# Kernel optimization log

Hardware: AMD Instinct MI355X
Metric: run time of the kernel (lower is better)

Reference implementation:

```python
import jax, jax.numpy as jnp
import numpy as np

NHID = 512
PROJ = 64          # fixed 64-dim projection from the source code
N_NODES = 16384
N_CLAIM = 4096
N_EVID = 8192
N_GRAPHS = 64


def setup_inputs() -> dict:
    key = jax.random.key(0)
    ks = jax.random.split(key, 10)
    x = jax.random.normal(ks[0], (N_NODES, NHID), dtype=jnp.float32)
    batch = jnp.sort(jax.random.randint(ks[1], (N_NODES,), 0, N_GRAPHS, dtype=jnp.int64))
    claim_index = jax.random.randint(ks[2], (N_CLAIM,), 0, N_NODES, dtype=jnp.int64)
    evidence_index = jax.random.randint(ks[3], (N_EVID,), 0, N_NODES, dtype=jnp.int64)
    # Linear params (PyTorch Linear: y = x @ W.T + b; store as [in, out] here)
    s_c = 1.0 / np.sqrt(NHID)
    Wc = jax.random.uniform(ks[4], (NHID, PROJ), jnp.float32, -s_c, s_c)
    bc = jax.random.uniform(ks[5], (PROJ,), jnp.float32, -s_c, s_c)
    We = jax.random.uniform(ks[6], (NHID, PROJ), jnp.float32, -s_c, s_c)
    be = jax.random.uniform(ks[7], (PROJ,), jnp.float32, -s_c, s_c)
    s_a = 1.0 / np.sqrt(4 * NHID)
    Wa = jax.random.uniform(ks[8], (4 * NHID, NHID), jnp.float32, -s_a, s_a)
    ba = jax.random.uniform(ks[9], (NHID,), jnp.float32, -s_a, s_a)
    return {"x": x, "batch": batch, "claim_index": claim_index,
            "evidence_index": evidence_index,
            "Wc": Wc, "bc": bc, "We": We, "be": be, "Wa": Wa, "ba": ba}


def reference(x, batch, claim_index, evidence_index, Wc, bc, We, be, Wa, ba):
    claim_batch = batch[claim_index]          # [Nc]
    evidence_batch = batch[evidence_index]    # [Ne]
    # block-diagonal mask: 0 where same graph, -inf otherwise
    same = claim_batch[:, None] == evidence_batch[None, :]
    mask = jnp.where(same, 0.0, -jnp.inf).astype(jnp.float32)  # [Nc, Ne]

    claim = x[claim_index]       # [Nc, nhid]
    evidence = x[evidence_index]  # [Ne, nhid]

    weight_c = claim @ Wc + bc    # [Nc, 64]
    weight_e = evidence @ We + be  # [Ne, 64]
    scores = weight_c @ weight_e.T + mask          # [Nc, Ne]
    attn = jax.nn.softmax(scores, axis=-1)
    claim_new = attn @ evidence                    # [Nc, nhid]

    a = jnp.concatenate([claim, claim_new, claim - claim_new, claim * claim_new], axis=-1)
    a = a @ Wa + ba               # [Nc, nhid]

    # global_mean_pool over claim_batch
    seg_sum = jax.ops.segment_sum(a, claim_batch, num_segments=N_GRAPHS)
    counts = jax.ops.segment_sum(jnp.ones((a.shape[0],), a.dtype), claim_batch,
                                 num_segments=N_GRAPHS)
    res = seg_sum / jnp.maximum(counts, 1.0)[:, None]  # [B, nhid]
    return res
```

## Files before the change

kernel.cpp:

```cpp
#include <hip/hip_runtime.h>
#include <hip/hip_bf16.h>

#define NHID 512
#define PROJ 64
#define NC 4096
#define NEV 8192
#define NG 64
#define NCMAX 128
#define NE_CAP 256
#define DSLICES 4
#define DW 128

typedef __attribute__((ext_vector_type(8))) short s16x8;
typedef __attribute__((ext_vector_type(8))) unsigned short u16x8;
typedef __attribute__((ext_vector_type(4))) float f32x4;

#define P_S_STRIDE 264
#define P_S_BYTES  (NCMAX * P_S_STRIDE * 2)
#define REGB_OFF   P_S_BYTES
#define WE_S_STRIDE 72
#define WC_S_OFF   (REGB_OFF + NE_CAP * WE_S_STRIDE * 2)
#define CN_S_STRIDE 132
#define MISC_OFF   (REGB_OFF + P_S_BYTES)
#define SMEM_BYTES (MISC_OFF + 1536)

static __device__ __forceinline__ unsigned short f2b(float f) {
  union { __hip_bfloat16 h; unsigned short u; } v;
  v.h = __float2bfloat16(f);
  return v.u;
}

template <int NPT>
__device__ __forceinline__ void compact_pairs(
    const int* __restrict__ batch, const int* __restrict__ idx, int g,
    int* __restrict__ off_out, int* __restrict__ cnt_out, int2* __restrict__ pairs) {
  __shared__ int wtot[4], wless[4];
  int t = threadIdx.x, lane = t & 63, w = t >> 6;
  int vals[NPT], nid[NPT];
  int base_i = t * NPT;
  int eq = 0, less = 0;
#pragma unroll
  for (int j = 0; j < NPT; j++) {
    int node = idx[base_i + j];
    int v = batch[node];
    vals[j] = v;
    nid[j] = node;
    eq += (v == g) ? 1 : 0;
    less += (v < g) ? 1 : 0;
  }
  int s = eq;
#pragma unroll
  for (int off = 1; off < 64; off <<= 1) {
    int o = __shfl_up(s, off);
    if (lane >= off) s += o;
  }
  int ls = less;
#pragma unroll
  for (int off = 32; off; off >>= 1) ls += __shfl_xor(ls, off);
  if (lane == 63) wtot[w] = s;
  if (lane == 0) wless[w] = ls;
  __syncthreads();
  int wbase = 0;
#pragma unroll
  for (int k = 0; k < 4; k++)
    if (k < w) wbase += wtot[k];
  int base = wless[0] + wless[1] + wless[2] + wless[3];
  int pos = base + wbase + (s - eq);
#pragma unroll
  for (int j = 0; j < NPT; j++) {
    if (vals[j] == g) pairs[pos++] = make_int2(base_i + j, nid[j]);
  }
  if (t == 255) {
    cnt_out[g] = wbase + s;
    off_out[g] = base;
  }
}

__global__ __launch_bounds__(256) void k_front(
    const float* __restrict__ Wc, const float* __restrict__ We,
    unsigned short* __restrict__ WcT, unsigned short* __restrict__ WeT,
    const int* __restrict__ batch, const int* __restrict__ cidx,
    const int* __restrict__ eidx, int* __restrict__ c_off, int* __restrict__ c_cnt,
    int2* __restrict__ c_pair, int* __restrict__ e_off, int* __restrict__ e_cnt,
    int2* __restrict__ e_pair) {
  int b = blockIdx.x;
  if (b < 16) {
    __shared__ float ts[64][65];
    const float* src = (b < 8) ? Wc : We;
    unsigned short* dst = (b < 8) ? WcT : WeT;
    int k0 = (b & 7) * 64;
    int t = threadIdx.x;
    int c = t & 63, r0 = t >> 6;
#pragma unroll
    for (int p = 0; p < 16; p++) {
      int r = r0 * 16 + p;
      ts[r][c] = src[(size_t)(k0 + r) * 64 + c];
    }
    __syncthreads();
    int n = t >> 2, q = t & 3;
    unsigned short tmp[16];
#pragma unroll
    for (int j = 0; j < 16; j++) tmp[j] = f2b(ts[q * 16 + j][n]);
    u16x8* dp = (u16x8*)(dst + (size_t)n * NHID + k0 + q * 16);
    dp[0] = *(u16x8*)tmp;
    dp[1] = *(u16x8*)(tmp + 8);
  } else if (b < 80) {
    compact_pairs<NC / 256>(batch, cidx, b - 16, c_off, c_cnt, c_pair);
  } else {
    compact_pairs<NEV / 256>(batch, eidx, b - 80, e_off, e_cnt, e_pair);
  }
}

__global__ __launch_bounds__(256) void k_proj(
    const float* __restrict__ x, const int* __restrict__ cidx,
    const int* __restrict__ eidx, const unsigned short* __restrict__ WcT,
    const unsigned short* __restrict__ WeT, const float* __restrict__ bc,
    const float* __restrict__ be, const float* __restrict__ Wa,
    unsigned short* __restrict__ WaT, unsigned short* __restrict__ wcp,
    unsigned short* __restrict__ wep) {
  __shared__ __align__(16) char sm[64 * 65 * 4];
  int b = blockIdx.x;
  int t = threadIdx.x;
  if (b >= 768) {
    int tb = b - 768;
    float(*ts)[65] = (float(*)[65])sm;
    int k0 = (tb >> 3) * 64, n0 = (tb & 7) * 64;
    int c = t & 63, r0 = t >> 6;
#pragma unroll
    for (int p = 0; p < 16; p++) {
      int r = r0 * 16 + p;
      ts[r][c] = Wa[(size_t)(k0 + r) * NHID + n0 + c];
    }
    __syncthreads();
    int n = t >> 2, q = t & 3;
    unsigned short tmp[16];
#pragma unroll
    for (int j = 0; j < 16; j++) tmp[j] = f2b(ts[q * 16 + j][n]);
    u16x8* dp = (u16x8*)(WaT + (size_t)(n0 + n) * (4 * NHID) + k0 + q * 16);
    dp[0] = *(u16x8*)tmp;
    dp[1] = *(u16x8*)(tmp + 8);
    return;
  }
  float(*red)[16][64] = (float(*)[16][64])sm;
  const int* idx; const unsigned short* WT; const float* bias;
  unsigned short* out; int base;
  if (b < NC / 16) { idx = cidx; WT = WcT; bias = bc; out = wcp; base = b * 16; }
  else             { idx = eidx; WT = WeT; bias = be; out = wep; base = (b - NC / 16) * 16; }
  int lane = t & 63, kh = t >> 6;
  int ln = lane & 15, kb = lane >> 4;
  const float* xr = x + (size_t)idx[base + ln] * NHID + kh * 128;
  const unsigned short* wb = WT + kh * 128;
  f32x4 acc[4];
#pragma unroll
  for (int nt = 0; nt < 4; nt++) acc[nt] = (f32x4){0.f, 0.f, 0.f, 0.f};
#pragma unroll
  for (int kt = 0; kt < 4; kt++) {
    int k0 = kt * 32 + kb * 8;
    float4 p0 = *(const float4*)(xr + k0);
    float4 p1 = *(const float4*)(xr + k0 + 4);
    s16x8 a;
    a[0] = (short)f2b(p0.x); a[1] = (short)f2b(p0.y);
    a[2] = (short)f2b(p0.z); a[3] = (short)f2b(p0.w);
    a[4] = (short)f2b(p1.x); a[5] = (short)f2b(p1.y);
    a[6] = (short)f2b(p1.z); a[7] = (short)f2b(p1.w);
#pragma unroll
    for (int nt = 0; nt < 4; nt++) {
      s16x8 bf = *(const s16x8*)(wb + (size_t)(nt * 16 + ln) * NHID + k0);
      acc[nt] = __builtin_amdgcn_mfma_f32_16x16x32_bf16(a, bf, acc[nt], 0, 0, 0);
    }
  }
#pragma unroll
  for (int nt = 0; nt < 4; nt++)
#pragma unroll
    for (int r = 0; r < 4; r++)
      red[kh][kb * 4 + r][nt * 16 + ln] = acc[nt][r];
  __syncthreads();
  for (int i = t; i < 512; i += 256) {
    int row = i >> 5, cp = i & 31;
    int c0 = cp * 2;
    float v0 = red[0][row][c0] + red[1][row][c0] + red[2][row][c0] + red[3][row][c0] + bias[c0];
    float v1 = red[0][row][c0 + 1] + red[1][row][c0 + 1] + red[2][row][c0 + 1] + red[3][row][c0 + 1] + bias[c0 + 1];
    unsigned int pk = (unsigned)f2b(v0) | ((unsigned)f2b(v1) << 16);
    *(unsigned int*)(out + (size_t)(base + row) * PROJ + c0) = pk;
  }
}

__global__ __launch_bounds__(512, 2) void k_attn(
    const float* __restrict__ x, const unsigned short* __restrict__ wcp,
    const unsigned short* __restrict__ wep, const int* __restrict__ c_off,
    const int* __restrict__ c_cnt, const int2* __restrict__ c_pair,
    const int* __restrict__ e_off, const int* __restrict__ e_cnt,
    const int2* __restrict__ e_pair, unsigned short* __restrict__ mcb) {
  __shared__ __align__(16) char smem[SMEM_BYTES];
  unsigned short* P_s  = (unsigned short*)(smem);
  unsigned short* we_s = (unsigned short*)(smem + REGB_OFF);
  unsigned short* wc_s = (unsigned short*)(smem + WC_S_OFF);
  unsigned short* evT  = (unsigned short*)(smem + REGB_OFF);
  unsigned int*   evT32 = (unsigned int*)(smem + REGB_OFF);
  float*          cn_s = (float*)(smem + REGB_OFF);
  float*          pp   = (float*)(smem);
  int* ev_id = (int*)(smem + MISC_OFF);
  int* cl_id = (int*)(smem + MISC_OFF + 1024);

  int g = blockIdx.x >> 2;
  int ds = blockIdx.x & 3;
  int dsbase = ds * DW;
  int t = threadIdx.x, lane = t & 63, w = t >> 6;
  int ln = lane & 15, kb = lane >> 4;

  int ne = min(e_cnt[g], NE_CAP);
  int eoff = e_off[g];
  int ccnt_full = c_cnt[g];
  int nloc = min(ccnt_full, NCMAX);
  int coff = c_off[g];
  if (nloc <= 0) {
    int q = t >> 7, d = t & 127;
    mcb[(size_t)g * 4 * NHID + q * NHID + dsbase + d] = 0;
    return;
  }
  int KT = (ne + 31) >> 5;
  int NT = KT * 2;

  for (int e = t; e < NE_CAP; e += 512)
    ev_id[e] = (e < ne) ? e_pair[eoff + e].y : 0;
  if (t < NCMAX) cl_id[t] = (t < nloc) ? c_pair[coff + t].y : 0;
  {
    int q = t & 7, er = t >> 3;
    for (int base_ = 0; base_ < NE_CAP; base_ += 64) {
      int e = base_ + er;
      u16x8 v = (u16x8){0, 0, 0, 0, 0, 0, 0, 0};
      if (e < ne) v = *(const u16x8*)(wep + (size_t)e_pair[eoff + e].x * PROJ + q * 8);
      *(u16x8*)(we_s + e * WE_S_STRIDE + q * 8) = v;
    }
    for (int base_ = 0; base_ < NCMAX; base_ += 64) {
      int c = base_ + er;
      u16x8 v = (u16x8){0, 0, 0, 0, 0, 0, 0, 0};
      if (c < nloc) v = *(const u16x8*)(wcp + (size_t)c_pair[coff + c].x * PROJ + q * 8);
      *(u16x8*)(wc_s + c * WE_S_STRIDE + q * 8) = v;
    }
  }
  __syncthreads();

  {
    f32x4 sa[16];
#pragma unroll
    for (int i = 0; i < 16; i++) sa[i] = (f32x4){0.f, 0.f, 0.f, 0.f};
    const unsigned short* arow = wc_s + ((w << 4) + ln) * WE_S_STRIDE;
#pragma unroll
    for (int ks = 0; ks < 2; ks++) {
      s16x8 af = *(const s16x8*)(arow + ks * 32 + kb * 8);
#pragma unroll
      for (int nt = 0; nt < 16; nt++) {
        if (nt < NT) {
          s16x8 bf = *(const s16x8*)(we_s + (nt * 16 + ln) * WE_S_STRIDE + ks * 32 + kb * 8);
          sa[nt] = __builtin_amdgcn_mfma_f32_16x16x32_bf16(af, bf, sa[nt], 0, 0, 0);
        }
      }
    }
#pragma unroll
    for (int r = 0; r < 4; r++) {
      int claim = (w << 4) + (kb << 2) + r;
      float mx = -1e30f;
#pragma unroll
      for (int nt = 0; nt < 16; nt++) {
        if (nt < NT) {
          float v = sa[nt][r];
          v = (nt * 16 + ln < ne) ? v : -1e30f;
          sa[nt][r] = v;
          mx = fmaxf(mx, v);
        }
      }
      mx = fmaxf(mx, __shfl_xor(mx, 1));
      mx = fmaxf(mx, __shfl_xor(mx, 2));
      mx = fmaxf(mx, __shfl_xor(mx, 4));
      mx = fmaxf(mx, __shfl_xor(mx, 8));
      float sum = 0.f;
#pragma unroll
      for (int nt = 0; nt < 16; nt++) {
        if (nt < NT) {
          float p = __expf(sa[nt][r] - mx);
          sa[nt][r] = p;
          sum += p;
        }
      }
      sum += __shfl_xor(sum, 1);
      sum += __shfl_xor(sum, 2);
      sum += __shfl_xor(sum, 4);
      sum += __shfl_xor(sum, 8);
      float inv = 1.f / sum;
#pragma unroll
      for (int nt = 0; nt < 16; nt++) {
        if (nt < NT)
          P_s[claim * P_S_STRIDE + nt * 16 + ln] = f2b(sa[nt][r] * inv);
      }
    }
  }
  __syncthreads();

#pragma unroll 4
  for (int pi = w; pi < NE_CAP / 2; pi += 8) {
    int e0 = pi * 2;
    float2 va = make_float2(0.f, 0.f);
    float2 vb = make_float2(0.f, 0.f);
    if (e0 < ne)     va = *(const float2*)(x + (size_t)ev_id[e0] * NHID + dsbase + 2 * lane);
    if (e0 + 1 < ne) vb = *(const float2*)(x + (size_t)ev_id[e0 + 1] * NHID + dsbase + 2 * lane);
    evT32[(2 * lane)     * (P_S_STRIDE / 2) + pi] = (unsigned)f2b(va.x) | ((unsigned)f2b(vb.x) << 16);
    evT32[(2 * lane + 1) * (P_S_STRIDE / 2) + pi] = (unsigned)f2b(va.y) | ((unsigned)f2b(vb.y) << 16);
  }
  __syncthreads();

  int dq4 = (t & 31) * 4;
  int mg = t >> 5;
  float4 cl_r[8];
#pragma unroll
  for (int mi = 0; mi < 8; mi++) {
    int m = mg + mi * 16;
    cl_r[mi] = make_float4(0.f, 0.f, 0.f, 0.f);
    if (m < nloc)
      cl_r[mi] = *(const float4*)(x + (size_t)cl_id[m] * NHID + dsbase + dq4);
  }

  int mw = w >> 1, nw = w & 1;
  int m0 = mw * 32, n0 = nw * 64;
  f32x4 pc[8];
#pragma unroll
  for (int i = 0; i < 8; i++) pc[i] = (f32x4){0.f, 0.f, 0.f, 0.f};
  {
    const unsigned short* prow0 = P_s + (m0 + ln) * P_S_STRIDE + kb * 8;
    const unsigned short* prow1 = prow0 + 16 * P_S_STRIDE;
#pragma unroll
    for (int kt = 0; kt < 8; kt++) {
      if (kt < KT) {
        int k0 = kt * 32;
        s16x8 a0 = *(const s16x8*)(prow0 + k0);
        s16x8 a1 = *(const s16x8*)(prow1 + k0);
#pragma unroll
        for (int nt = 0; nt < 4; nt++) {
          s16x8 bf = *(const s16x8*)(evT + (n0 + nt * 16 + ln) * P_S_STRIDE + k0 + kb * 8);
          pc[nt]     = __builtin_amdgcn_mfma_f32_16x16x32_bf16(a0, bf, pc[nt], 0, 0, 0);
          pc[4 + nt] = __builtin_amdgcn_mfma_f32_16x16x32_bf16(a1, bf, pc[4 + nt], 0, 0, 0);
        }
      }
    }
  }
  __syncthreads();

#pragma unroll
  for (int mi = 0; mi < 2; mi++) {
#pragma unroll
    for (int nt = 0; nt < 4; nt++) {
      f32x4 v = pc[mi * 4 + nt];
#pragma unroll
      for (int r = 0; r < 4; r++)
        cn_s[(m0 + mi * 16 + (kb << 2) + r) * CN_S_STRIDE + n0 + nt * 16 + ln] = v[r];
    }
  }
  __syncthreads();

  {
    float4 scl = make_float4(0.f, 0.f, 0.f, 0.f);
    float4 scn = make_float4(0.f, 0.f, 0.f, 0.f);
    float4 spr = make_float4(0.f, 0.f, 0.f, 0.f);
#pragma unroll
    for (int mi = 0; mi < 8; mi++) {
      int m = mg + mi * 16;
      if (m < nloc) {
        float4 cl = cl_r[mi];
        float4 cn = *(const float4*)(cn_s + m * CN_S_STRIDE + dq4);
        scl.x += cl.x; scl.y += cl.y; scl.z += cl.z; scl.w += cl.w;
        scn.x += cn.x; scn.y += cn.y; scn.z += cn.z; scn.w += cn.w;
        spr.x += cl.x * cn.x; spr.y += cl.y * cn.y;
        spr.z += cl.z * cn.z; spr.w += cl.w * cn.w;
      }
    }
    *(float4*)(pp + mg * 128 + dq4) = scl;
    *(float4*)(pp + 2048 + mg * 128 + dq4) = scn;
    *(float4*)(pp + 4096 + mg * 128 + dq4) = spr;
  }
  __syncthreads();

  {
    int q = t >> 7, d = t & 127;
    float inv = 1.f / (float)max(ccnt_full, 1);
    float v = 0.f;
    if (q == 0) {
#pragma unroll
      for (int mg2 = 0; mg2 < 16; mg2++) v += pp[mg2 * 128 + d];
    } else if (q == 1) {
#pragma unroll
      for (int mg2 = 0; mg2 < 16; mg2++) v += pp[2048 + mg2 * 128 + d];
    } else if (q == 2) {
#pragma unroll
      for (int mg2 = 0; mg2 < 16; mg2++) v += pp[mg2 * 128 + d] - pp[2048 + mg2 * 128 + d];
    } else {
#pragma unroll
      for (int mg2 = 0; mg2 < 16; mg2++) v += pp[4096 + mg2 * 128 + d];
    }
    mcb[(size_t)g * 4 * NHID + q * NHID + dsbase + d] = f2b(v * inv);
  }
}

__global__ __launch_bounds__(512) void k_out(
    const unsigned short* __restrict__ mc, const unsigned short* __restrict__ WaT,
    const float* __restrict__ ba, float* __restrict__ out) {
  __shared__ float red[2][64][16];
  int n0 = blockIdx.x * 16;
  int t = threadIdx.x, lane = t & 63, wv = t >> 6;
  int mh = wv & 3, kh = wv >> 2;
  int ln = lane & 15, kb = lane >> 4;
  f32x4 acc = (f32x4){0.f, 0.f, 0.f, 0.f};
  const unsigned short* arow = mc + (size_t)(mh * 16 + ln) * (4 * NHID) + kh * 1024;
  const unsigned short* wcol = WaT + (size_t)(n0 + ln) * (4 * NHID) + kh * 1024;
#pragma unroll 4
  for (int kt = 0; kt < 32; kt++) {
    int k0 = kt * 32 + kb * 8;
    s16x8 af = *(const s16x8*)(arow + k0);
    s16x8 bf = *(const s16x8*)(wcol + k0);
    acc = __builtin_amdgcn_mfma_f32_16x16x32_bf16(af, bf, acc, 0, 0, 0);
  }
#pragma unroll
  for (int r = 0; r < 4; r++)
    red[kh][mh * 16 + kb * 4 + r][ln] = acc[r];
  __syncthreads();
  for (int i = t; i < 1024; i += 512) {
    int row = i >> 4, col = i & 15;
    out[(size_t)row * NHID + n0 + col] = red[0][row][col] + red[1][row][col] + ba[n0 + col];
  }
}

extern "C" void kernel_launch(void* const* d_in, const int* in_sizes, int n_in,
                              void* d_out, int out_size, void* d_ws, size_t ws_size,
                              hipStream_t stream) {
  const float* x = (const float*)d_in[0];
  const int* batch = (const int*)d_in[1];
  const int* cidx = (const int*)d_in[2];
  const int* eidx = (const int*)d_in[3];
  const float* Wc = (const float*)d_in[4];
  const float* bc = (const float*)d_in[5];
  const float* We = (const float*)d_in[6];
  const float* be = (const float*)d_in[7];
  const float* Wa = (const float*)d_in[8];
  const float* ba = (const float*)d_in[9];
  float* out = (float*)d_out;

  char* w = (char*)d_ws;
  int* c_off = (int*)w;    w += NG * 4;
  int* c_cnt = (int*)w;    w += NG * 4;
  int* e_off = (int*)w;    w += NG * 4;
  int* e_cnt = (int*)w;    w += NG * 4;
  int2* c_pair = (int2*)w; w += (size_t)NC * 8;
  int2* e_pair = (int2*)w; w += (size_t)NEV * 8;
  unsigned short* wcp = (unsigned short*)w; w += (size_t)NC * PROJ * 2;
  unsigned short* wep = (unsigned short*)w; w += (size_t)NEV * PROJ * 2;
  unsigned short* WcT = (unsigned short*)w; w += (size_t)PROJ * NHID * 2;
  unsigned short* WeT = (unsigned short*)w; w += (size_t)PROJ * NHID * 2;
  unsigned short* WaT = (unsigned short*)w; w += (size_t)NHID * 4 * NHID * 2;
  unsigned short* mcb = (unsigned short*)w; w += (size_t)NG * 4 * NHID * 2;

  k_front<<<144, 256, 0, stream>>>(Wc, We, WcT, WeT, batch, cidx, eidx,
                                   c_off, c_cnt, c_pair, e_off, e_cnt, e_pair);
  k_proj<<<768 + 256, 256, 0, stream>>>(x, cidx, eidx, WcT, WeT, bc, be, Wa, WaT,
                                        wcp, wep);
  k_attn<<<NG * DSLICES, 512, 0, stream>>>(x, wcp, wep, c_off, c_cnt, c_pair,
                                           e_off, e_cnt, e_pair, mcb);
  k_out<<<32, 512, 0, stream>>>(mcb, WaT, ba, out);
}
```

Measured before the change: 61.91 us.

## Write graph-sorted bf16 copies of gathered rows in proj, read contiguously in attn

The projection kernel now walks the rows in compacted per-graph order and, while projecting, also writes the bf16-converted claim and evidence rows into contiguous per-graph buffers. The attention kernel then reads these contiguous bf16 rows with 16-byte vector loads instead of doing indirect fp32 gathers from x through index tables. This removes the index tables from shared memory and halves the bytes read in attention. In exchange, proj writes about 12 MB of extra bf16 data, and the claim values used in the elementwise terms are now bf16-rounded instead of fp32.

```diff
diff --git a/kernel.cpp b/kernel.cpp
--- a/kernel.cpp
+++ b/kernel.cpp
@@ -21,13 +21,17 @@
 #define WE_S_STRIDE 72
 #define WC_S_OFF   (REGB_OFF + NE_CAP * WE_S_STRIDE * 2)
 #define CN_S_STRIDE 132
-#define MISC_OFF   (REGB_OFF + P_S_BYTES)
-#define SMEM_BYTES (MISC_OFF + 1536)
+#define SMEM_BYTES (REGB_OFF + P_S_BYTES)
 
 static __device__ __forceinline__ unsigned short f2b(float f) {
   union { __hip_bfloat16 h; unsigned short u; } v;
   v.h = __float2bfloat16(f);
   return v.u;
+}
+static __device__ __forceinline__ float b2f(unsigned short u) {
+  union { unsigned short u; __hip_bfloat16 h; } v;
+  v.u = u;
+  return __bfloat162float(v.h);
 }
 
 template <int NPT>
@@ -112,12 +116,13 @@
 }
 
 __global__ __launch_bounds__(256) void k_proj(
-    const float* __restrict__ x, const int* __restrict__ cidx,
-    const int* __restrict__ eidx, const unsigned short* __restrict__ WcT,
+    const float* __restrict__ x, const int2* __restrict__ c_pair,
+    const int2* __restrict__ e_pair, const unsigned short* __restrict__ WcT,
     const unsigned short* __restrict__ WeT, const float* __restrict__ bc,
     const float* __restrict__ be, const float* __restrict__ Wa,
-    unsigned short* __restrict__ WaT, unsigned short* __restrict__ wcp,
-    unsigned short* __restrict__ wep) {
+    unsigned short* __restrict__ WaT, unsigned short* __restrict__ wcp_c,
+    unsigned short* __restrict__ wep_c, unsigned short* __restrict__ xc_c,
+    unsigned short* __restrict__ xe_c) {
   __shared__ __align__(16) char sm[64 * 65 * 4];
   int b = blockIdx.x;
   int t = threadIdx.x;
@@ -142,13 +147,14 @@
     return;
   }
   float(*red)[16][64] = (float(*)[16][64])sm;
-  const int* idx; const unsigned short* WT; const float* bias;
-  unsigned short* out; int base;
-  if (b < NC / 16) { idx = cidx; WT = WcT; bias = bc; out = wcp; base = b * 16; }
-  else             { idx = eidx; WT = WeT; bias = be; out = wep; base = (b - NC / 16) * 16; }
+  const int2* pair; const unsigned short* WT; const float* bias;
+  unsigned short* out; unsigned short* xout; int base;
+  if (b < NC / 16) { pair = c_pair; WT = WcT; bias = bc; out = wcp_c; xout = xc_c; base = b * 16; }
+  else             { pair = e_pair; WT = WeT; bias = be; out = wep_c; xout = xe_c; base = (b - NC / 16) * 16; }
   int lane = t & 63, kh = t >> 6;
   int ln = lane & 15, kb = lane >> 4;
-  const float* xr = x + (size_t)idx[base + ln] * NHID + kh * 128;
+  const float* xr = x + (size_t)pair[base + ln].y * NHID + kh * 128;
+  unsigned short* xw = xout + (size_t)(base + ln) * NHID + kh * 128;
   const unsigned short* wb = WT + kh * 128;
   f32x4 acc[4];
 #pragma unroll
@@ -163,6 +169,7 @@
     a[2] = (short)f2b(p0.z); a[3] = (short)f2b(p0.w);
     a[4] = (short)f2b(p1.x); a[5] = (short)f2b(p1.y);
     a[6] = (short)f2b(p1.z); a[7] = (short)f2b(p1.w);
+    *(u16x8*)(xw + k0) = (u16x8)a;
 #pragma unroll
     for (int nt = 0; nt < 4; nt++) {
       s16x8 bf = *(const s16x8*)(wb + (size_t)(nt * 16 + ln) * NHID + k0);
@@ -186,11 +193,11 @@
 }
 
 __global__ __launch_bounds__(512, 2) void k_attn(
-    const float* __restrict__ x, const unsigned short* __restrict__ wcp,
-    const unsigned short* __restrict__ wep, const int* __restrict__ c_off,
-    const int* __restrict__ c_cnt, const int2* __restrict__ c_pair,
+    const unsigned short* __restrict__ xc_c, const unsigned short* __restrict__ xe_c,
+    const unsigned short* __restrict__ wcp_c, const unsigned short* __restrict__ wep_c,
+    const int* __restrict__ c_off, const int* __restrict__ c_cnt,
     const int* __restrict__ e_off, const int* __restrict__ e_cnt,
-    const int2* __restrict__ e_pair, unsigned short* __restrict__ mcb) {
+    unsigned short* __restrict__ mcb) {
   __shared__ __align__(16) char smem[SMEM_BYTES];
   unsigned short* P_s  = (unsigned short*)(smem);
   unsigned short* we_s = (unsigned short*)(smem + REGB_OFF);
@@ -199,8 +206,6 @@
   unsigned int*   evT32 = (unsigned int*)(smem + REGB_OFF);
   float*          cn_s = (float*)(smem + REGB_OFF);
   float*          pp   = (float*)(smem);
-  int* ev_id = (int*)(smem + MISC_OFF);
-  int* cl_id = (int*)(smem + MISC_OFF + 1024);
 
   int g = blockIdx.x >> 2;
   int ds = blockIdx.x & 3;
@@ -221,21 +226,18 @@
   int KT = (ne + 31) >> 5;
   int NT = KT * 2;
 
-  for (int e = t; e < NE_CAP; e += 512)
-    ev_id[e] = (e < ne) ? e_pair[eoff + e].y : 0;
-  if (t < NCMAX) cl_id[t] = (t < nloc) ? c_pair[coff + t].y : 0;
   {
     int q = t & 7, er = t >> 3;
     for (int base_ = 0; base_ < NE_CAP; base_ += 64) {
       int e = base_ + er;
       u16x8 v = (u16x8){0, 0, 0, 0, 0, 0, 0, 0};
-      if (e < ne) v = *(const u16x8*)(wep + (size_t)e_pair[eoff + e].x * PROJ + q * 8);
+      if (e < ne) v = *(const u16x8*)(wep_c + (size_t)(eoff + e) * PROJ + q * 8);
       *(u16x8*)(we_s + e * WE_S_STRIDE + q * 8) = v;
     }
     for (int base_ = 0; base_ < NCMAX; base_ += 64) {
       int c = base_ + er;
       u16x8 v = (u16x8){0, 0, 0, 0, 0, 0, 0, 0};
-      if (c < nloc) v = *(const u16x8*)(wcp + (size_t)c_pair[coff + c].x * PROJ + q * 8);
+      if (c < nloc) v = *(const u16x8*)(wcp_c + (size_t)(coff + c) * PROJ + q * 8);
       *(u16x8*)(wc_s + c * WE_S_STRIDE + q * 8) = v;
     }
   }
@@ -297,27 +299,33 @@
   }
   __syncthreads();
 
-#pragma unroll 4
-  for (int pi = w; pi < NE_CAP / 2; pi += 8) {
-    int e0 = pi * 2;
-    float2 va = make_float2(0.f, 0.f);
-    float2 vb = make_float2(0.f, 0.f);
-    if (e0 < ne)     va = *(const float2*)(x + (size_t)ev_id[e0] * NHID + dsbase + 2 * lane);
-    if (e0 + 1 < ne) vb = *(const float2*)(x + (size_t)ev_id[e0 + 1] * NHID + dsbase + 2 * lane);
-    evT32[(2 * lane)     * (P_S_STRIDE / 2) + pi] = (unsigned)f2b(va.x) | ((unsigned)f2b(vb.x) << 16);
-    evT32[(2 * lane + 1) * (P_S_STRIDE / 2) + pi] = (unsigned)f2b(va.y) | ((unsigned)f2b(vb.y) << 16);
+#pragma unroll
+  for (int it = 0; it < 4; it++) {
+    int idx2 = it * 512 + t;
+    int ep = ((idx2 >> 7) << 3) | (idx2 & 7);
+    int j8 = (idx2 >> 3) & 15;
+    int d0 = j8 * 8;
+    int e0 = ep * 2;
+    u16x8 va = (u16x8){0, 0, 0, 0, 0, 0, 0, 0};
+    u16x8 vb = (u16x8){0, 0, 0, 0, 0, 0, 0, 0};
+    if (e0 < ne)     va = *(const u16x8*)(xe_c + (size_t)(eoff + e0) * NHID + dsbase + d0);
+    if (e0 + 1 < ne) vb = *(const u16x8*)(xe_c + (size_t)(eoff + e0 + 1) * NHID + dsbase + d0);
+#pragma unroll
+    for (int j = 0; j < 8; j++)
+      evT32[(d0 + j) * (P_S_STRIDE / 2) + ep] =
+          (unsigned)(unsigned short)va[j] | ((unsigned)(unsigned short)vb[j] << 16);
   }
   __syncthreads();
 
   int dq4 = (t & 31) * 4;
   int mg = t >> 5;
-  float4 cl_r[8];
+  ushort4 cl_u[8];
 #pragma unroll
   for (int mi = 0; mi < 8; mi++) {
     int m = mg + mi * 16;
-    cl_r[mi] = make_float4(0.f, 0.f, 0.f, 0.f);
+    cl_u[mi] = make_ushort4(0, 0, 0, 0);
     if (m < nloc)
-      cl_r[mi] = *(const float4*)(x + (size_t)cl_id[m] * NHID + dsbase + dq4);
+      cl_u[mi] = *(const ushort4*)(xc_c + (size_t)(coff + m) * NHID + dsbase + dq4);
   }
 
   int mw = w >> 1, nw = w & 1;
@@ -365,12 +373,13 @@
     for (int mi = 0; mi < 8; mi++) {
       int m = mg + mi * 16;
       if (m < nloc) {
-        float4 cl = cl_r[mi];
+        float clx = b2f(cl_u[mi].x), cly = b2f(cl_u[mi].y);
+        float clz = b2f(cl_u[mi].z), clw = b2f(cl_u[mi].w);
         float4 cn = *(const float4*)(cn_s + m * CN_S_STRIDE + dq4);
-        scl.x += cl.x; scl.y += cl.y; scl.z += cl.z; scl.w += cl.w;
+        scl.x += clx; scl.y += cly; scl.z += clz; scl.w += clw;
         scn.x += cn.x; scn.y += cn.y; scn.z += cn.z; scn.w += cn.w;
-        spr.x += cl.x * cn.x; spr.y += cl.y * cn.y;
-        spr.z += cl.z * cn.z; spr.w += cl.w * cn.w;
+        spr.x += clx * cn.x; spr.y += cly * cn.y;
+        spr.z += clz * cn.z; spr.w += clw * cn.w;
       }
     }
     *(float4*)(pp + mg * 128 + dq4) = scl;
@@ -450,18 +459,20 @@
   int* e_cnt = (int*)w;    w += NG * 4;
   int2* c_pair = (int2*)w; w += (size_t)NC * 8;
   int2* e_pair = (int2*)w; w += (size_t)NEV * 8;
-  unsigned short* wcp = (unsigned short*)w; w += (size_t)NC * PROJ * 2;
-  unsigned short* wep = (unsigned short*)w; w += (size_t)NEV * PROJ * 2;
-  unsigned short* WcT = (unsigned short*)w; w += (size_t)PROJ * NHID * 2;
-  unsigned short* WeT = (unsigned short*)w; w += (size_t)PROJ * NHID * 2;
-  unsigned short* WaT = (unsigned short*)w; w += (size_t)NHID * 4 * NHID * 2;
-  unsigned short* mcb = (unsigned short*)w; w += (size_t)NG * 4 * NHID * 2;
+  unsigned short* wcp_c = (unsigned short*)w; w += (size_t)NC * PROJ * 2;
+  unsigned short* wep_c = (unsigned short*)w; w += (size_t)NEV * PROJ * 2;
+  unsigned short* WcT = (unsigned short*)w;   w += (size_t)PROJ * NHID * 2;
+  unsigned short* WeT = (unsigned short*)w;   w += (size_t)PROJ * NHID * 2;
+  unsigned short* WaT = (unsigned short*)w;   w += (size_t)NHID * 4 * NHID * 2;
+  unsigned short* mcb = (unsigned short*)w;   w += (size_t)NG * 4 * NHID * 2;
+  unsigned short* xc_c = (unsigned short*)w;  w += (size_t)NC * NHID * 2;
+  unsigned short* xe_c = (unsigned short*)w;  w += (size_t)NEV * NHID * 2;
 
   k_front<<<144, 256, 0, stream>>>(Wc, We, WcT, WeT, batch, cidx, eidx,
                                    c_off, c_cnt, c_pair, e_off, e_cnt, e_pair);
-  k_proj<<<768 + 256, 256, 0, stream>>>(x, cidx, eidx, WcT, WeT, bc, be, Wa, WaT,
-                                        wcp, wep);
-  k_attn<<<NG * DSLICES, 512, 0, stream>>>(x, wcp, wep, c_off, c_cnt, c_pair,
-                                           e_off, e_cnt, e_pair, mcb);
+  k_proj<<<768 + 256, 256, 0, stream>>>(x, c_pair, e_pair, WcT, WeT, bc, be, Wa, WaT,
+                                        wcp_c, wep_c, xc_c, xe_c);
+  k_attn<<<NG * DSLICES, 512, 0, stream>>>(xc_c, xe_c, wcp_c, wep_c,
+                                           c_off, c_cnt, e_off, e_cnt, mcb);
   k_out<<<32, 512, 0, stream>>>(mcb, WaT, ba, out);
 }
```

Result: faster. 56.84 us (median of 2 runs) (-8.2%).
